# Kernel optimization log

Hardware: AMD Instinct MI355X
Metric: run time of the kernel (lower is better)

The kernel has to match this reference:

```python
import jax, jax.numpy as jnp
import numpy as np
from jax import lax

K = 31      # avg_pool kernel
PAD = 15    # padding (count_include_pad=True -> divide by K*K always)
LAMBDA1 = 1.0
LAMBDA2 = 1.0


def _box_mean(x):
    # 31x31 stride-1 avg pool with zero padding, divisor = K*K (torch default count_include_pad=True)
    s = lax.reduce_window(x, 0.0, lax.add, (1, 1, K, K), (1, 1, 1, 1),
                          [(0, 0), (0, 0), (PAD, PAD), (PAD, PAD)])
    return s / float(K * K)


def setup_inputs() -> dict:
    key = jax.random.key(0)
    k1, k2 = jax.random.split(key)
    pred = jax.random.normal(k1, (64, 1, 512, 512), dtype=jnp.float32)
    mask = jax.random.uniform(k2, (64, 1, 512, 512), dtype=jnp.float32)
    return {"pred": pred, "mask": mask}


def reference(pred, mask):
    weit = 1.0 + 5.0 * jnp.abs(_box_mean(mask) - mask)
    # bce_with_logits, numerically stable: max(x,0) - x*y + log1p(exp(-|x|))
    bce = jnp.maximum(pred, 0.0) - pred * mask + jnp.log1p(jnp.exp(-jnp.abs(pred)))
    # NOTE: original torch code passes reduce='none' (deprecated kwarg, truthy string),
    # which resolves to reduction='mean' -> wbce is a SCALAR; the (weit*.)/weit.sum
    # normalization then cancels exactly. We reproduce that behavior faithfully.
    wbce = jnp.mean(bce)  # scalar, broadcast over (B, C)
    p = jax.nn.sigmoid(pred)
    inter = jnp.sum(p * mask * weit, axis=(2, 3))       # [B, C]
    union = jnp.sum((p + mask) * weit, axis=(2, 3))     # [B, C]
    wiou = 1.0 - (inter + 1.0) / (union - inter + 1.0)  # [B, C]
    return jnp.mean(LAMBDA1 * wbce + LAMBDA2 * wiou)
```

## Files before the change

kernel.cpp:

```cpp
#include <hip/hip_runtime.h>
#include <math.h>

#define BATCH 64
#define HH 512
#define WW 512
#define PAD 15
#define NELEM ((size_t)BATCH * HH * WW)
#define INV_KK (1.0f / 961.0f)

#define TILE_H 16
#define BPI (HH / TILE_H)
#define NBLK (BATCH * BPI)
#define NXCD 8

typedef float f4 __attribute__((ext_vector_type(4)));

__device__ __forceinline__ float wave_reduce(float v) {
    #pragma unroll
    for (int off = 32; off; off >>= 1) v += __shfl_down(v, off, 64);
    return v;
}

__global__ __launch_bounds__(256) void fused_kernel(const float* __restrict__ pred,
                                                    const float* __restrict__ mask,
                                                    double* __restrict__ partials) {
    __shared__ float vrow[4][WW];
    __shared__ float P[4][WW];
    __shared__ float red[3][4];

    const int f    = blockIdx.x;
    const int xcd  = f & (NXCD - 1);
    const int slot = f >> 3;
    const int img  = xcd * 8 + (slot >> 5);
    const int tile = slot & (BPI - 1);

    const int tid  = threadIdx.x;
    const int lane = tid & 63;
    const int wv   = tid >> 6;
    const int h0   = tile * TILE_H;
    const int c0   = tid;
    const int c1   = tid + 256;

    const float* mb = mask + (size_t)img * HH * WW;
    const float* pb = pred + (size_t)img * HH * WW;

    float r0 = 0.0f, r1 = 0.0f;
    {
        int lo = h0 - PAD; if (lo < 0) lo = 0;
        int hi = h0 + PAD; if (hi > HH - 1) hi = HH - 1;
        for (int y = lo; y <= hi; ++y) {
            r0 += mb[(size_t)y * WW + c0];
            r1 += mb[(size_t)y * WW + c1];
        }
    }

    float accb = 0.0f, acci = 0.0f, accu = 0.0f;

    #pragma unroll 1
    for (int it = 0; it < TILE_H / 4; ++it) {
        const int hbase = h0 + it * 4;

        #pragma unroll
        for (int j = 0; j < 4; ++j) {
            const int h = hbase + j;
            vrow[j][c0] = r0;
            vrow[j][c1] = r1;
            const int add = h + PAD + 1;
            const int sub = h - PAD;
            float a0 = 0.0f, a1 = 0.0f, s0 = 0.0f, s1 = 0.0f;
            if (add < HH) { a0 = mb[(size_t)add * WW + c0]; a1 = mb[(size_t)add * WW + c1]; }
            if (sub >= 0) { s0 = mb[(size_t)sub * WW + c0]; s1 = mb[(size_t)sub * WW + c1]; }
            r0 += a0 - s0;
            r1 += a1 - s1;
        }
        __syncthreads();

        const int h = hbase + wv;
        const size_t rbase = (size_t)h * WW;

        f4 va = *(const f4*)&vrow[wv][8 * lane];
        f4 vb = *(const f4*)&vrow[wv][8 * lane + 4];
        float p0 = va.x;
        float p1 = p0 + va.y;
        float p2 = p1 + va.z;
        float p3 = p2 + va.w;
        float p4 = p3 + vb.x;
        float p5 = p4 + vb.y;
        float p6 = p5 + vb.z;
        float p7 = p6 + vb.w;
        float lanesum = p7;
        float incl = lanesum;
        #pragma unroll
        for (int off = 1; off < 64; off <<= 1) {
            float n = __shfl_up(incl, off, 64);
            if (lane >= off) incl += n;
        }
        const float excl = incl - lanesum;
        f4 Pa, Pb;
        Pa.x = excl + p0; Pa.y = excl + p1; Pa.z = excl + p2; Pa.w = excl + p3;
        Pb.x = excl + p4; Pb.y = excl + p5; Pb.z = excl + p6; Pb.w = excl + p7;
        *(f4*)&P[wv][8 * lane]     = Pa;
        *(f4*)&P[wv][8 * lane + 4] = Pb;

        #pragma unroll
        for (int k = 0; k < 8; ++k) {
            const int w = lane + 64 * k;
            int hiw = w + PAD; if (hiw > WW - 1) hiw = WW - 1;
            float s = P[wv][hiw];
            if (w >= PAD + 1) s -= P[wv][w - PAD - 1];

            const float m  = mb[rbase + w];
            const float pr = pb[rbase + w];

            const float weit = 1.0f + 5.0f * fabsf(s * INV_KK - m);
            const float e    = __expf(-fabsf(pr));
            const float bce  = fmaxf(pr, 0.0f) - pr * m + __logf(1.0f + e);
            const float inv  = __builtin_amdgcn_rcpf(1.0f + e);
            const float p    = (pr >= 0.0f) ? inv : e * inv;

            accb += bce;
            acci += p * m * weit;
            accu += (p + m) * weit;
        }
        __syncthreads();
    }

    accb = wave_reduce(accb);
    acci = wave_reduce(acci);
    accu = wave_reduce(accu);
    if (lane == 0) { red[0][wv] = accb; red[1][wv] = acci; red[2][wv] = accu; }
    __syncthreads();
    if (tid == 0) {
        double bt = (double)red[0][0] + red[0][1] + red[0][2] + red[0][3];
        double it2 = (double)red[1][0] + red[1][1] + red[1][2] + red[1][3];
        double ut = (double)red[2][0] + red[2][1] + red[2][2] + red[2][3];
        const size_t pidx = (size_t)img * BPI + tile;
        partials[pidx * 3 + 0] = bt;
        partials[pidx * 3 + 1] = it2;
        partials[pidx * 3 + 2] = ut;
    }
}

__global__ __launch_bounds__(256) void finalize_kernel(const double* __restrict__ partials,
                                                       float* __restrict__ out) {
    __shared__ double redbce[4];
    int tid = threadIdx.x, lane = tid & 63, wv = tid >> 6;

    double bsum = 0.0;
    for (int i = tid; i < NBLK; i += 256) bsum += partials[(size_t)i * 3 + 0];
    #pragma unroll
    for (int off = 32; off; off >>= 1) bsum += __shfl_down(bsum, off, 64);
    if (lane == 0) redbce[wv] = bsum;
    __syncthreads();

    double wiou_term = 0.0;
    if (tid < 64) {
        int bb = tid;
        double it = 0.0, ut = 0.0;
        for (int j = 0; j < BPI; ++j) {
            it += partials[(size_t)(bb * BPI + j) * 3 + 1];
            ut += partials[(size_t)(bb * BPI + j) * 3 + 2];
        }
        wiou_term = 1.0 - (it + 1.0) / (ut - it + 1.0);
    }
    if (wv == 0) {
        #pragma unroll
        for (int off = 32; off; off >>= 1) wiou_term += __shfl_down(wiou_term, off, 64);
    }
    if (tid == 0) {
        double wbce = (redbce[0] + redbce[1] + redbce[2] + redbce[3]) / (double)NELEM;
        out[0] = (float)(wbce + wiou_term * (1.0 / 64.0));
    }
}

#define ACC_DOUBLES 129
__global__ __launch_bounds__(256) void rowpass_nows_kernel(const float* __restrict__ pred,
                                                           const float* __restrict__ mask,
                                                           double* __restrict__ acc) {
    __shared__ float vrow1[WW];
    __shared__ float red[3][4];
    int b = blockIdx.x / HH;
    int h = blockIdx.x % HH;
    int lo = h - PAD; if (lo < 0) lo = 0;
    int hi = h + PAD; if (hi > HH - 1) hi = HH - 1;
    float s0 = 0.0f, s1 = 0.0f;
    const float* mb = mask + (size_t)b * HH * WW;
    for (int y = lo; y <= hi; ++y) {
        s0 += mb[(size_t)y * WW + threadIdx.x];
        s1 += mb[(size_t)y * WW + threadIdx.x + 256];
    }
    vrow1[threadIdx.x]       = s0;
    vrow1[threadIdx.x + 256] = s1;
    __syncthreads();

    size_t base = ((size_t)b * HH + h) * WW;
    float bce_p = 0.0f, inter_p = 0.0f, uni_p = 0.0f;
    for (int w = threadIdx.x; w < WW; w += 256) {
        int wlo = w - PAD; if (wlo < 0) wlo = 0;
        int whi = w + PAD; if (whi > WW - 1) whi = WW - 1;
        float s = 0.0f;
        for (int k = wlo; k <= whi; ++k) s += vrow1[k];
        float m  = mask[base + w];
        float pr = pred[base + w];
        float weit = 1.0f + 5.0f * fabsf(s * INV_KK - m);
        float e   = expf(-fabsf(pr));
        float bce = fmaxf(pr, 0.0f) - pr * m + log1pf(e);
        float inv = 1.0f / (1.0f + e);
        float p   = (pr >= 0.0f) ? inv : e * inv;
        bce_p += bce; inter_p += p * m * weit; uni_p += (p + m) * weit;
    }
    int lane = threadIdx.x & 63, wvv = threadIdx.x >> 6;
    bce_p = wave_reduce(bce_p); inter_p = wave_reduce(inter_p); uni_p = wave_reduce(uni_p);
    if (lane == 0) { red[0][wvv] = bce_p; red[1][wvv] = inter_p; red[2][wvv] = uni_p; }
    __syncthreads();
    if (threadIdx.x == 0) {
        atomicAdd(&acc[0], (double)(red[0][0] + red[0][1] + red[0][2] + red[0][3]));
        atomicAdd(&acc[1 + b], (double)(red[1][0] + red[1][1] + red[1][2] + red[1][3]));
        atomicAdd(&acc[65 + b], (double)(red[2][0] + red[2][1] + red[2][2] + red[2][3]));
    }
}

__global__ void finalize_atomic_kernel(const double* __restrict__ acc, float* __restrict__ out) {
    int b = threadIdx.x;
    double inter = acc[1 + b];
    double uni   = acc[65 + b];
    double wiou = 1.0 - (inter + 1.0) / (uni - inter + 1.0);
    #pragma unroll
    for (int off = 32; off; off >>= 1) wiou += __shfl_down(wiou, off, 64);
    if (b == 0) {
        double wbce = acc[0] / (double)NELEM;
        out[0] = (float)(wbce + wiou * (1.0 / 64.0));
    }
}

extern "C" void kernel_launch(void* const* d_in, const int* in_sizes, int n_in,
                              void* d_out, int out_size, void* d_ws, size_t ws_size,
                              hipStream_t stream) {
    const float* pred = (const float*)d_in[0];
    const float* mask = (const float*)d_in[1];
    float* out = (float*)d_out;

    const size_t part_bytes = (size_t)NBLK * 3 * sizeof(double);

    if (ws_size >= part_bytes) {
        double* partials = (double*)d_ws;
        fused_kernel<<<NBLK, 256, 0, stream>>>(pred, mask, partials);
        finalize_kernel<<<1, 256, 0, stream>>>(partials, out);
    } else {
        double* acc = (double*)d_ws;
        hipMemsetAsync(acc, 0, ACC_DOUBLES * sizeof(double), stream);
        rowpass_nows_kernel<<<BATCH * HH, 256, 0, stream>>>(pred, mask, acc);
        finalize_atomic_kernel<<<1, 64, 0, stream>>>(acc, out);
    }
}
```

Before: 61.63 us.

## Software-pipeline global loads with double-buffered vrow and taller row tiles

Prefetches the next iteration's mask/pred row values and the running-column add/subtract rows into registers while the current iteration computes, ping-ponging two register sets. vrow is double-buffered so the second barrier per iteration can be dropped. The tile height doubles to 32, which halves the block count and the column-sum warmup overhead per output row. The cost is higher register pressure and less parallelism from fewer blocks.

```diff
diff --git a/kernel.cpp b/kernel.cpp
--- a/kernel.cpp
+++ b/kernel.cpp
@@ -8,7 +8,9 @@
 #define NELEM ((size_t)BATCH * HH * WW)
 #define INV_KK (1.0f / 961.0f)
 
-#define TILE_H 16
+#define TILE_H 32
+#define RPI 4
+#define NIT (TILE_H / RPI)
 #define BPI (HH / TILE_H)
 #define NBLK (BATCH * BPI)
 #define NXCD 8
@@ -21,17 +23,100 @@
     return v;
 }
 
+__device__ __forceinline__ void iter_body(
+    int it, int h0, int lane, int wv, int c0, int c1,
+    float& r0, float& r1,
+    float (&pa)[RPI], float (&ps)[RPI], float (&qa)[RPI], float (&qs)[RPI],
+    float (&mc)[8], float (&pc)[8], float (&mn)[8], float (&pn)[8],
+    const float* __restrict__ mb, const float* __restrict__ pb,
+    float (*vb)[WW], float* __restrict__ Prow,
+    float& accb, float& acci, float& accu)
+{
+    #pragma unroll
+    for (int j = 0; j < RPI; ++j) {
+        vb[j][c0] = r0;
+        vb[j][c1] = r1;
+        r0 += pa[j] - ps[j];
+        r1 += qa[j] - qs[j];
+    }
+    __syncthreads();
+
+    if (it + 1 < NIT) {
+        const int hb = h0 + RPI * (it + 1);
+        #pragma unroll
+        for (int j = 0; j < RPI; ++j) {
+            const int ar = hb + 16 + j;
+            const int sr = hb - 15 + j;
+            pa[j] = (ar < HH) ? mb[(size_t)ar * WW + c0] : 0.0f;
+            qa[j] = (ar < HH) ? mb[(size_t)ar * WW + c1] : 0.0f;
+            ps[j] = (sr >= 0) ? mb[(size_t)sr * WW + c0] : 0.0f;
+            qs[j] = (sr >= 0) ? mb[(size_t)sr * WW + c1] : 0.0f;
+        }
+        const size_t rbn = (size_t)(hb + wv) * WW;
+        #pragma unroll
+        for (int k = 0; k < 8; ++k) {
+            mn[k] = mb[rbn + lane + 64 * k];
+            pn[k] = pb[rbn + lane + 64 * k];
+        }
+    }
+
+    f4 va = *(const f4*)&vb[wv][8 * lane];
+    f4 vc = *(const f4*)&vb[wv][8 * lane + 4];
+    float p0 = va.x;
+    float p1 = p0 + va.y;
+    float p2 = p1 + va.z;
+    float p3 = p2 + va.w;
+    float p4 = p3 + vc.x;
+    float p5 = p4 + vc.y;
+    float p6 = p5 + vc.z;
+    float p7 = p6 + vc.w;
+    float lanesum = p7;
+    float incl = lanesum;
+    #pragma unroll
+    for (int off = 1; off < 64; off <<= 1) {
+        float n = __shfl_up(incl, off, 64);
+        if (lane >= off) incl += n;
+    }
+    const float excl = incl - lanesum;
+    f4 Pa, Pb;
+    Pa.x = excl + p0; Pa.y = excl + p1; Pa.z = excl + p2; Pa.w = excl + p3;
+    Pb.x = excl + p4; Pb.y = excl + p5; Pb.z = excl + p6; Pb.w = excl + p7;
+    *(f4*)&Prow[8 * lane]     = Pa;
+    *(f4*)&Prow[8 * lane + 4] = Pb;
+
+    #pragma unroll
+    for (int k = 0; k < 8; ++k) {
+        const int w = lane + 64 * k;
+        int hiw = w + PAD; if (hiw > WW - 1) hiw = WW - 1;
+        float s = Prow[hiw];
+        if (w >= PAD + 1) s -= Prow[w - PAD - 1];
+
+        const float m  = mc[k];
+        const float pr = pc[k];
+
+        const float weit = 1.0f + 5.0f * fabsf(s * INV_KK - m);
+        const float e    = __expf(-fabsf(pr));
+        const float bce  = fmaxf(pr, 0.0f) - pr * m + __logf(1.0f + e);
+        const float inv  = __builtin_amdgcn_rcpf(1.0f + e);
+        const float p    = (pr >= 0.0f) ? inv : e * inv;
+
+        accb += bce;
+        acci += p * m * weit;
+        accu += (p + m) * weit;
+    }
+}
+
 __global__ __launch_bounds__(256) void fused_kernel(const float* __restrict__ pred,
                                                     const float* __restrict__ mask,
                                                     double* __restrict__ partials) {
-    __shared__ float vrow[4][WW];
+    __shared__ float vrow[2][RPI][WW];
     __shared__ float P[4][WW];
     __shared__ float red[3][4];
 
     const int f    = blockIdx.x;
     const int xcd  = f & (NXCD - 1);
     const int slot = f >> 3;
-    const int img  = xcd * 8 + (slot >> 5);
+    const int img  = xcd * 8 + (slot >> 4);
     const int tile = slot & (BPI - 1);
 
     const int tid  = threadIdx.x;
@@ -54,75 +139,38 @@
         }
     }
 
+    float pa[RPI], ps[RPI], qa[RPI], qs[RPI];
+    float mc[8], pc[8], mn[8], pn[8];
+
+    {
+        const int hb = h0;
+        #pragma unroll
+        for (int j = 0; j < RPI; ++j) {
+            const int ar = hb + 16 + j;
+            const int sr = hb - 15 + j;
+            pa[j] = (ar < HH) ? mb[(size_t)ar * WW + c0] : 0.0f;
+            qa[j] = (ar < HH) ? mb[(size_t)ar * WW + c1] : 0.0f;
+            ps[j] = (sr >= 0) ? mb[(size_t)sr * WW + c0] : 0.0f;
+            qs[j] = (sr >= 0) ? mb[(size_t)sr * WW + c1] : 0.0f;
+        }
+        const size_t rb0 = (size_t)(h0 + wv) * WW;
+        #pragma unroll
+        for (int k = 0; k < 8; ++k) {
+            mc[k] = mb[rb0 + lane + 64 * k];
+            pc[k] = pb[rb0 + lane + 64 * k];
+        }
+    }
+
     float accb = 0.0f, acci = 0.0f, accu = 0.0f;
 
     #pragma unroll 1
-    for (int it = 0; it < TILE_H / 4; ++it) {
-        const int hbase = h0 + it * 4;
-
-        #pragma unroll
-        for (int j = 0; j < 4; ++j) {
-            const int h = hbase + j;
-            vrow[j][c0] = r0;
-            vrow[j][c1] = r1;
-            const int add = h + PAD + 1;
-            const int sub = h - PAD;
-            float a0 = 0.0f, a1 = 0.0f, s0 = 0.0f, s1 = 0.0f;
-            if (add < HH) { a0 = mb[(size_t)add * WW + c0]; a1 = mb[(size_t)add * WW + c1]; }
-            if (sub >= 0) { s0 = mb[(size_t)sub * WW + c0]; s1 = mb[(size_t)sub * WW + c1]; }
-            r0 += a0 - s0;
-            r1 += a1 - s1;
-        }
-        __syncthreads();
-
-        const int h = hbase + wv;
-        const size_t rbase = (size_t)h * WW;
-
-        f4 va = *(const f4*)&vrow[wv][8 * lane];
-        f4 vb = *(const f4*)&vrow[wv][8 * lane + 4];
-        float p0 = va.x;
-        float p1 = p0 + va.y;
-        float p2 = p1 + va.z;
-        float p3 = p2 + va.w;
-        float p4 = p3 + vb.x;
-        float p5 = p4 + vb.y;
-        float p6 = p5 + vb.z;
-        float p7 = p6 + vb.w;
-        float lanesum = p7;
-        float incl = lanesum;
-        #pragma unroll
-        for (int off = 1; off < 64; off <<= 1) {
-            float n = __shfl_up(incl, off, 64);
-            if (lane >= off) incl += n;
-        }
-        const float excl = incl - lanesum;
-        f4 Pa, Pb;
-        Pa.x = excl + p0; Pa.y = excl + p1; Pa.z = excl + p2; Pa.w = excl + p3;
-        Pb.x = excl + p4; Pb.y = excl + p5; Pb.z = excl + p6; Pb.w = excl + p7;
-        *(f4*)&P[wv][8 * lane]     = Pa;
-        *(f4*)&P[wv][8 * lane + 4] = Pb;
-
-        #pragma unroll
-        for (int k = 0; k < 8; ++k) {
-            const int w = lane + 64 * k;
-            int hiw = w + PAD; if (hiw > WW - 1) hiw = WW - 1;
-            float s = P[wv][hiw];
-            if (w >= PAD + 1) s -= P[wv][w - PAD - 1];
-
-            const float m  = mb[rbase + w];
-            const float pr = pb[rbase + w];
-
-            const float weit = 1.0f + 5.0f * fabsf(s * INV_KK - m);
-            const float e    = __expf(-fabsf(pr));
-            const float bce  = fmaxf(pr, 0.0f) - pr * m + __logf(1.0f + e);
-            const float inv  = __builtin_amdgcn_rcpf(1.0f + e);
-            const float p    = (pr >= 0.0f) ? inv : e * inv;
-
-            accb += bce;
-            acci += p * m * weit;
-            accu += (p + m) * weit;
-        }
-        __syncthreads();
+    for (int i2 = 0; i2 < NIT / 2; ++i2) {
+        iter_body(2 * i2,     h0, lane, wv, c0, c1, r0, r1,
+                  pa, ps, qa, qs, mc, pc, mn, pn,
+                  mb, pb, vrow[0], P[wv], accb, acci, accu);
+        iter_body(2 * i2 + 1, h0, lane, wv, c0, c1, r0, r1,
+                  pa, ps, qa, qs, mn, pn, mc, pc,
+                  mb, pb, vrow[1], P[wv], accb, acci, accu);
     }
 
     accb = wave_reduce(accb);
```

Result: no change. 61.66 us (+0.0%).

## Give each wave its own row strip with register vertical sums, dropping block barriers

Applied to the files above, without the earlier changes.

Each wave now owns 8 consecutive rows and keeps 8 per-lane vertical running sums in registers, loaded as float4. Before, the whole block built vertical sums in a shared vrow buffer and needed two __syncthreads per 4 rows. Without that buffer and those barriers, waves advance independently through prefix scan, box sum and loss math. The cost is a 31-row warm-up per wave instead of per block, which adds redundant mask reads. Tile height also doubles to 32, halving the block count. Shared P row reuse within a wave now relies on the wave executing in lockstep, with no barrier.

```diff
diff --git a/kernel.cpp b/kernel.cpp
--- a/kernel.cpp
+++ b/kernel.cpp
@@ -8,7 +8,8 @@
 #define NELEM ((size_t)BATCH * HH * WW)
 #define INV_KK (1.0f / 961.0f)
 
-#define TILE_H 16
+#define RPW 8
+#define TILE_H 32
 #define BPI (HH / TILE_H)
 #define NBLK (BATCH * BPI)
 #define NXCD 8
@@ -24,90 +25,73 @@
 __global__ __launch_bounds__(256) void fused_kernel(const float* __restrict__ pred,
                                                     const float* __restrict__ mask,
                                                     double* __restrict__ partials) {
-    __shared__ float vrow[4][WW];
     __shared__ float P[4][WW];
     __shared__ float red[3][4];
 
     const int f    = blockIdx.x;
     const int xcd  = f & (NXCD - 1);
     const int slot = f >> 3;
-    const int img  = xcd * 8 + (slot >> 5);
-    const int tile = slot & (BPI - 1);
+    const int img  = xcd * 8 + (slot >> 4);
+    const int t    = slot & (BPI - 1);
 
     const int tid  = threadIdx.x;
     const int lane = tid & 63;
     const int wv   = tid >> 6;
-    const int h0   = tile * TILE_H;
-    const int c0   = tid;
-    const int c1   = tid + 256;
+    const int h0   = t * TILE_H + wv * RPW;
+    const int c    = 8 * lane;
 
     const float* mb = mask + (size_t)img * HH * WW;
     const float* pb = pred + (size_t)img * HH * WW;
 
-    float r0 = 0.0f, r1 = 0.0f;
+    float r0 = 0.f, r1 = 0.f, r2 = 0.f, r3 = 0.f, r4 = 0.f, r5 = 0.f, r6 = 0.f, r7 = 0.f;
     {
         int lo = h0 - PAD; if (lo < 0) lo = 0;
         int hi = h0 + PAD; if (hi > HH - 1) hi = HH - 1;
         for (int y = lo; y <= hi; ++y) {
-            r0 += mb[(size_t)y * WW + c0];
-            r1 += mb[(size_t)y * WW + c1];
+            f4 m0 = *(const f4*)&mb[(size_t)y * WW + c];
+            f4 m1 = *(const f4*)&mb[(size_t)y * WW + c + 4];
+            r0 += m0.x; r1 += m0.y; r2 += m0.z; r3 += m0.w;
+            r4 += m1.x; r5 += m1.y; r6 += m1.z; r7 += m1.w;
         }
     }
 
     float accb = 0.0f, acci = 0.0f, accu = 0.0f;
+    float* Prow = P[wv];
 
     #pragma unroll 1
-    for (int it = 0; it < TILE_H / 4; ++it) {
-        const int hbase = h0 + it * 4;
-
-        #pragma unroll
-        for (int j = 0; j < 4; ++j) {
-            const int h = hbase + j;
-            vrow[j][c0] = r0;
-            vrow[j][c1] = r1;
-            const int add = h + PAD + 1;
-            const int sub = h - PAD;
-            float a0 = 0.0f, a1 = 0.0f, s0 = 0.0f, s1 = 0.0f;
-            if (add < HH) { a0 = mb[(size_t)add * WW + c0]; a1 = mb[(size_t)add * WW + c1]; }
-            if (sub >= 0) { s0 = mb[(size_t)sub * WW + c0]; s1 = mb[(size_t)sub * WW + c1]; }
-            r0 += a0 - s0;
-            r1 += a1 - s1;
-        }
-        __syncthreads();
-
-        const int h = hbase + wv;
+    for (int j = 0; j < RPW; ++j) {
+        const int h = h0 + j;
         const size_t rbase = (size_t)h * WW;
 
-        f4 va = *(const f4*)&vrow[wv][8 * lane];
-        f4 vb = *(const f4*)&vrow[wv][8 * lane + 4];
-        float p0 = va.x;
-        float p1 = p0 + va.y;
-        float p2 = p1 + va.z;
-        float p3 = p2 + va.w;
-        float p4 = p3 + vb.x;
-        float p5 = p4 + vb.y;
-        float p6 = p5 + vb.z;
-        float p7 = p6 + vb.w;
-        float lanesum = p7;
-        float incl = lanesum;
+        const float p0 = r0;
+        const float p1 = p0 + r1;
+        const float p2 = p1 + r2;
+        const float p3 = p2 + r3;
+        const float p4 = p3 + r4;
+        const float p5 = p4 + r5;
+        const float p6 = p5 + r6;
+        const float p7 = p6 + r7;
+
+        float incl = p7;
         #pragma unroll
         for (int off = 1; off < 64; off <<= 1) {
             float n = __shfl_up(incl, off, 64);
             if (lane >= off) incl += n;
         }
-        const float excl = incl - lanesum;
+        const float excl = incl - p7;
+
         f4 Pa, Pb;
         Pa.x = excl + p0; Pa.y = excl + p1; Pa.z = excl + p2; Pa.w = excl + p3;
         Pb.x = excl + p4; Pb.y = excl + p5; Pb.z = excl + p6; Pb.w = excl + p7;
-        *(f4*)&P[wv][8 * lane]     = Pa;
-        *(f4*)&P[wv][8 * lane + 4] = Pb;
+        *(f4*)&Prow[c]     = Pa;
+        *(f4*)&Prow[c + 4] = Pb;
 
         #pragma unroll
         for (int k = 0; k < 8; ++k) {
             const int w = lane + 64 * k;
             int hiw = w + PAD; if (hiw > WW - 1) hiw = WW - 1;
-            float s = P[wv][hiw];
-            if (w >= PAD + 1) s -= P[wv][w - PAD - 1];
+            float s = Prow[hiw];
+            if (w >= PAD + 1) s -= Prow[w - PAD - 1];
 
             const float m  = mb[rbase + w];
             const float pr = pb[rbase + w];
@@ -122,7 +106,21 @@
             acci += p * m * weit;
             accu += (p + m) * weit;
         }
-        __syncthreads();
+
+        const int add = h + PAD + 1;
+        const int sub = h - PAD;
+        if (add < HH) {
+            f4 a0 = *(const f4*)&mb[(size_t)add * WW + c];
+            f4 a1 = *(const f4*)&mb[(size_t)add * WW + c + 4];
+            r0 += a0.x; r1 += a0.y; r2 += a0.z; r3 += a0.w;
+            r4 += a1.x; r5 += a1.y; r6 += a1.z; r7 += a1.w;
+        }
+        if (sub >= 0) {
+            f4 s0 = *(const f4*)&mb[(size_t)sub * WW + c];
+            f4 s1 = *(const f4*)&mb[(size_t)sub * WW + c + 4];
+            r0 -= s0.x; r1 -= s0.y; r2 -= s0.z; r3 -= s0.w;
+            r4 -= s1.x; r5 -= s1.y; r6 -= s1.z; r7 -= s1.w;
+        }
     }
 
     accb = wave_reduce(accb);
@@ -134,7 +132,7 @@
         double bt = (double)red[0][0] + red[0][1] + red[0][2] + red[0][3];
         double it2 = (double)red[1][0] + red[1][1] + red[1][2] + red[1][3];
         double ut = (double)red[2][0] + red[2][1] + red[2][2] + red[2][3];
-        const size_t pidx = (size_t)img * BPI + tile;
+        const size_t pidx = (size_t)img * BPI + t;
         partials[pidx * 3 + 0] = bt;
         partials[pidx * 3 + 1] = it2;
         partials[pidx * 3 + 2] = ut;
```

Result: slower. 70.46 us (+14.3%).
